# Kernel tuning notes

Hardware: AMD Instinct MI355X
Metric: run time of the kernel (lower is better)

The kernel has to match this reference:

```python
import jax, jax.numpy as jnp
import numpy as np

D_MODEL = 3072
NUM_EXPERTS = 8
TOP_K = 2
BATCH, SEQ = 4, 4096


def setup_inputs() -> dict:
    key = jax.random.key(0)
    kx, kw, kb = jax.random.split(key, 3)
    x = jax.random.normal(kx, (BATCH, SEQ, D_MODEL), dtype=jnp.float32)
    W = jax.random.normal(kw, (NUM_EXPERTS, D_MODEL), dtype=jnp.float32) * (1.0 / np.sqrt(D_MODEL))
    b = jax.random.normal(kb, (NUM_EXPERTS,), dtype=jnp.float32) * 0.02
    return {"x": x, "W": W, "b": b}


def reference(x, W, b):
    # Linear gate: [B, S, D] x [E, D]^T -> [B, S, E]
    logits = jnp.einsum("bsd,ed->bse", x, W) + b
    gate_scores = jax.nn.softmax(logits, axis=-1)
    # top-k over experts
    topk_values, topk_indices = jax.lax.top_k(gate_scores, TOP_K)
    # renormalize the selected scores with a second softmax
    topk_values = jax.nn.softmax(topk_values, axis=-1)
    return (topk_values, topk_indices)
```

## Files before the change

### kernel.cpp

```cpp
#include <hip/hip_runtime.h>
#include <stdint.h>


#define NTOK   16384
#define DMODEL 3072
#define NEXP   8
#define TPB    256
#define TOKB   16
#define NST    48
#define NSS    12

__global__ __launch_bounds__(TPB) void gate_fused_kernel(
    const float* __restrict__ x, const float* __restrict__ W,
    const float* __restrict__ bias, float* __restrict__ out) {
  const int tid = threadIdx.x;
  const int wv = tid >> 6;
  const int lane = tid & 63;
  const int tg = lane & 3;
  const int sl = lane >> 2;
  const int tok = blockIdx.x * TOKB + wv * 4 + tg;

  const float* px = x + (size_t)tok * DMODEL + sl * 4;
  const float* pw[NEXP];
#pragma unroll
  for (int e = 0; e < NEXP; ++e) pw[e] = W + (size_t)e * DMODEL + sl * 4;

  float acc[NEXP];
#pragma unroll
  for (int e = 0; e < NEXP; ++e) acc[e] = 0.f;

  float4 xa[4], xb[4];
#pragma unroll
  for (int k = 0; k < 4; ++k) xa[k] = *(const float4*)(px + k * 64);

#pragma unroll 1
  for (int ss = 0; ss < NSS; ss += 2) {
#pragma unroll
    for (int k = 0; k < 4; ++k)
      xb[k] = *(const float4*)(px + ((ss + 1) * 4 + k) * 64);

#pragma unroll
    for (int k = 0; k < 4; ++k) {
      const int s = ss * 4 + k;
      float4 w4[NEXP];
#pragma unroll
      for (int e = 0; e < NEXP; ++e)
        w4[e] = *(const float4*)(pw[e] + s * 64);
      const float4 xv = xa[k];
#pragma unroll
      for (int e = 0; e < NEXP; ++e)
        acc[e] = fmaf(xv.x, w4[e].x,
                 fmaf(xv.y, w4[e].y,
                 fmaf(xv.z, w4[e].z,
                 fmaf(xv.w, w4[e].w, acc[e]))));
    }

    if (ss + 2 < NSS) {
#pragma unroll
      for (int k = 0; k < 4; ++k)
        xa[k] = *(const float4*)(px + ((ss + 2) * 4 + k) * 64);
    }

#pragma unroll
    for (int k = 0; k < 4; ++k) {
      const int s = (ss + 1) * 4 + k;
      float4 w4[NEXP];
#pragma unroll
      for (int e = 0; e < NEXP; ++e)
        w4[e] = *(const float4*)(pw[e] + s * 64);
      const float4 xv = xb[k];
#pragma unroll
      for (int e = 0; e < NEXP; ++e)
        acc[e] = fmaf(xv.x, w4[e].x,
                 fmaf(xv.y, w4[e].y,
                 fmaf(xv.z, w4[e].z,
                 fmaf(xv.w, w4[e].w, acc[e]))));
    }
  }

#pragma unroll
  for (int e = 0; e < NEXP; ++e) {
    float v = acc[e];
    v += __shfl_xor(v, 4, 64);
    v += __shfl_xor(v, 8, 64);
    v += __shfl_xor(v, 16, 64);
    v += __shfl_xor(v, 32, 64);
    acc[e] = v;
  }

  const float4 b0 = *(const float4*)bias;
  const float4 b1 = *(const float4*)(bias + 4);
  float l[NEXP];
  l[0] = acc[0] + b0.x; l[1] = acc[1] + b0.y;
  l[2] = acc[2] + b0.z; l[3] = acc[3] + b0.w;
  l[4] = acc[4] + b1.x; l[5] = acc[5] + b1.y;
  l[6] = acc[6] + b1.z; l[7] = acc[7] + b1.w;

  float m = l[0];
#pragma unroll
  for (int e = 1; e < NEXP; ++e) m = fmaxf(m, l[e]);

  float p8[NEXP];
  float ssum = 0.f;
#pragma unroll
  for (int e = 0; e < NEXP; ++e) {
    p8[e] = expf(l[e] - m);
    ssum += p8[e];
  }
  const float inv = 1.f / ssum;
#pragma unroll
  for (int e = 0; e < NEXP; ++e) p8[e] *= inv;

  int i1 = 0;
  float v1 = p8[0];
#pragma unroll
  for (int e = 1; e < NEXP; ++e) {
    if (p8[e] > v1) { v1 = p8[e]; i1 = e; }
  }
  int i2 = -1;
  float v2 = -1.f;
#pragma unroll
  for (int e = 0; e < NEXP; ++e) {
    if (e == i1) continue;
    if (p8[e] > v2) { v2 = p8[e]; i2 = e; }
  }

  const float e2 = expf(v2 - v1);
  const float r = 1.f / (1.f + e2);

  if (lane < 4) {
    *(float2*)(out + (size_t)tok * 2) = make_float2(r, e2 * r);
    *(float2*)(out + 2 * NTOK + (size_t)tok * 2) =
        make_float2((float)i1, (float)i2);
  }
}

extern "C" void kernel_launch(void* const* d_in, const int* in_sizes, int n_in,
                              void* d_out, int out_size, void* d_ws,
                              size_t ws_size, hipStream_t stream) {
  const float* x = (const float*)d_in[0];
  const float* W = (const float*)d_in[1];
  const float* b = (const float*)d_in[2];
  float* out = (float*)d_out;
  (void)d_ws; (void)ws_size;

  gate_fused_kernel<<<dim3(NTOK / TOKB), TPB, 0, stream>>>(x, W, b, out);
}
```

Measured before the change: 307.2 us.

## Stage gate weights in double-buffered LDS and compute 8 tokens per wave

Weight chunks of 256 features for all 8 experts are now loaded cooperatively into double-buffered shared memory, with the next chunk prefetched while the current one is used. Each wave now processes 8 tokens instead of 4, and each thread accumulates four tokens, so every weight value read from LDS is reused across several tokens. This is meant to cut repeated global/L2 weight reads per token. In exchange it adds block barriers, more accumulator and x-prefetch registers, which may lower occupancy, and a longer shuffle reduction.

```diff
diff --git a/kernel.cpp b/kernel.cpp
--- a/kernel.cpp
+++ b/kernel.cpp
@@ -6,132 +6,173 @@
 #define DMODEL 3072
 #define NEXP   8
 #define TPB    256
-#define TOKB   16
-#define NST    48
-#define NSS    12
+#define TOKW   8
+#define TOKB   32
+#define CHF    256
+#define NCH    (DMODEL / CHF)
+#define LDSF   (NEXP * CHF)
 
-__global__ __launch_bounds__(TPB) void gate_fused_kernel(
+#define GATE_COMPUTE(SW, XR)                                          \
+  {                                                                   \
+    _Pragma("unroll")                                                 \
+    for (int st = 0; st < 2; ++st) {                                  \
+      float4 w4[NEXP];                                                \
+      _Pragma("unroll")                                               \
+      for (int e = 0; e < NEXP; ++e)                                  \
+        w4[e] = *(const float4*)&SW[e * CHF + st * 128 + sl * 4];     \
+      _Pragma("unroll")                                               \
+      for (int p = 0; p < 4; ++p) {                                   \
+        const float4 xv = XR[st * 4 + p];                             \
+        _Pragma("unroll")                                             \
+        for (int e = 0; e < NEXP; ++e)                                \
+          acc[p][e] = fmaf(xv.x, w4[e].x,                             \
+                      fmaf(xv.y, w4[e].y,                             \
+                      fmaf(xv.z, w4[e].z,                             \
+                      fmaf(xv.w, w4[e].w, acc[p][e]))));              \
+      }                                                               \
+    }                                                                 \
+  }
+
+__global__ __launch_bounds__(TPB) void gate_fused2(
     const float* __restrict__ x, const float* __restrict__ W,
     const float* __restrict__ bias, float* __restrict__ out) {
-  const int tid = threadIdx.x;
-  const int wv = tid >> 6;
+  __shared__ float swA[LDSF];
+  __shared__ float swB[LDSF];
+
+  const int tid  = threadIdx.x;
+  const int wv   = tid >> 6;
   const int lane = tid & 63;
-  const int tg = lane & 3;
-  const int sl = lane >> 2;
-  const int tok = blockIdx.x * TOKB + wv * 4 + tg;
+  const int tg   = lane & 1;
+  const int sl   = lane >> 1;
+  const int tokBase = blockIdx.x * TOKB + wv * TOKW;
 
-  const float* px = x + (size_t)tok * DMODEL + sl * 4;
-  const float* pw[NEXP];
+  const float* px[4];
 #pragma unroll
-  for (int e = 0; e < NEXP; ++e) pw[e] = W + (size_t)e * DMODEL + sl * 4;
+  for (int p = 0; p < 4; ++p)
+    px[p] = x + (size_t)(tokBase + p * 2 + tg) * DMODEL + sl * 4;
 
-  float acc[NEXP];
+  const float* pw0 = W + (size_t)wv * DMODEL + (tid & 63) * 4;
+  const float* pw1 = W + (size_t)(4 + wv) * DMODEL + (tid & 63) * 4;
+  const int d0 = tid * 4;
+  const int d1 = 1024 + tid * 4;
+
+  float acc[4][NEXP];
 #pragma unroll
-  for (int e = 0; e < NEXP; ++e) acc[e] = 0.f;
+  for (int p = 0; p < 4; ++p)
+#pragma unroll
+    for (int e = 0; e < NEXP; ++e) acc[p][e] = 0.f;
 
-  float4 xa[4], xb[4];
+  float4 w0 = *(const float4*)(pw0);
+  float4 w1 = *(const float4*)(pw1);
+  float4 xa[8], xb[8];
 #pragma unroll
-  for (int k = 0; k < 4; ++k) xa[k] = *(const float4*)(px + k * 64);
+  for (int st = 0; st < 2; ++st)
+#pragma unroll
+    for (int p = 0; p < 4; ++p)
+      xa[st * 4 + p] = *(const float4*)(px[p] + st * 128);
+  *(float4*)&swA[d0] = w0;
+  *(float4*)&swA[d1] = w1;
+  __syncthreads();
 
 #pragma unroll 1
-  for (int ss = 0; ss < NSS; ss += 2) {
+  for (int cc = 0; cc < NCH; cc += 2) {
+    w0 = *(const float4*)(pw0 + (cc + 1) * CHF);
+    w1 = *(const float4*)(pw1 + (cc + 1) * CHF);
 #pragma unroll
-    for (int k = 0; k < 4; ++k)
-      xb[k] = *(const float4*)(px + ((ss + 1) * 4 + k) * 64);
+    for (int st = 0; st < 2; ++st)
+#pragma unroll
+      for (int p = 0; p < 4; ++p)
+        xb[st * 4 + p] =
+            *(const float4*)(px[p] + ((cc + 1) * 2 + st) * 128);
 
+    GATE_COMPUTE(swA, xa);
+
+    *(float4*)&swB[d0] = w0;
+    *(float4*)&swB[d1] = w1;
+    __syncthreads();
+
+    if (cc + 2 < NCH) {
+      w0 = *(const float4*)(pw0 + (cc + 2) * CHF);
+      w1 = *(const float4*)(pw1 + (cc + 2) * CHF);
 #pragma unroll
-    for (int k = 0; k < 4; ++k) {
-      const int s = ss * 4 + k;
-      float4 w4[NEXP];
+      for (int st = 0; st < 2; ++st)
 #pragma unroll
-      for (int e = 0; e < NEXP; ++e)
-        w4[e] = *(const float4*)(pw[e] + s * 64);
-      const float4 xv = xa[k];
-#pragma unroll
-      for (int e = 0; e < NEXP; ++e)
-        acc[e] = fmaf(xv.x, w4[e].x,
-                 fmaf(xv.y, w4[e].y,
-                 fmaf(xv.z, w4[e].z,
-                 fmaf(xv.w, w4[e].w, acc[e]))));
+        for (int p = 0; p < 4; ++p)
+          xa[st * 4 + p] =
+              *(const float4*)(px[p] + ((cc + 2) * 2 + st) * 128);
     }
 
-    if (ss + 2 < NSS) {
-#pragma unroll
-      for (int k = 0; k < 4; ++k)
-        xa[k] = *(const float4*)(px + ((ss + 2) * 4 + k) * 64);
+    GATE_COMPUTE(swB, xb);
+
+    if (cc + 2 < NCH) {
+      *(float4*)&swA[d0] = w0;
+      *(float4*)&swA[d1] = w1;
     }
-
-#pragma unroll
-    for (int k = 0; k < 4; ++k) {
-      const int s = (ss + 1) * 4 + k;
-      float4 w4[NEXP];
-#pragma unroll
-      for (int e = 0; e < NEXP; ++e)
-        w4[e] = *(const float4*)(pw[e] + s * 64);
-      const float4 xv = xb[k];
-#pragma unroll
-      for (int e = 0; e < NEXP; ++e)
-        acc[e] = fmaf(xv.x, w4[e].x,
-                 fmaf(xv.y, w4[e].y,
-                 fmaf(xv.z, w4[e].z,
-                 fmaf(xv.w, w4[e].w, acc[e]))));
-    }
+    __syncthreads();
   }
 
 #pragma unroll
-  for (int e = 0; e < NEXP; ++e) {
-    float v = acc[e];
-    v += __shfl_xor(v, 4, 64);
-    v += __shfl_xor(v, 8, 64);
-    v += __shfl_xor(v, 16, 64);
-    v += __shfl_xor(v, 32, 64);
-    acc[e] = v;
-  }
+  for (int p = 0; p < 4; ++p)
+#pragma unroll
+    for (int e = 0; e < NEXP; ++e) {
+      float v = acc[p][e];
+      v += __shfl_xor(v, 2, 64);
+      v += __shfl_xor(v, 4, 64);
+      v += __shfl_xor(v, 8, 64);
+      v += __shfl_xor(v, 16, 64);
+      v += __shfl_xor(v, 32, 64);
+      acc[p][e] = v;
+    }
 
   const float4 b0 = *(const float4*)bias;
   const float4 b1 = *(const float4*)(bias + 4);
-  float l[NEXP];
-  l[0] = acc[0] + b0.x; l[1] = acc[1] + b0.y;
-  l[2] = acc[2] + b0.z; l[3] = acc[3] + b0.w;
-  l[4] = acc[4] + b1.x; l[5] = acc[5] + b1.y;
-  l[6] = acc[6] + b1.z; l[7] = acc[7] + b1.w;
 
-  float m = l[0];
 #pragma unroll
-  for (int e = 1; e < NEXP; ++e) m = fmaxf(m, l[e]);
+  for (int p = 0; p < 4; ++p) {
+    if (sl == p) {
+      float l[NEXP];
+      l[0] = acc[p][0] + b0.x; l[1] = acc[p][1] + b0.y;
+      l[2] = acc[p][2] + b0.z; l[3] = acc[p][3] + b0.w;
+      l[4] = acc[p][4] + b1.x; l[5] = acc[p][5] + b1.y;
+      l[6] = acc[p][6] + b1.z; l[7] = acc[p][7] + b1.w;
 
-  float p8[NEXP];
-  float ssum = 0.f;
+      float m = l[0];
 #pragma unroll
-  for (int e = 0; e < NEXP; ++e) {
-    p8[e] = expf(l[e] - m);
-    ssum += p8[e];
-  }
-  const float inv = 1.f / ssum;
+      for (int e = 1; e < NEXP; ++e) m = fmaxf(m, l[e]);
+
+      float p8[NEXP];
+      float ssum = 0.f;
 #pragma unroll
-  for (int e = 0; e < NEXP; ++e) p8[e] *= inv;
+      for (int e = 0; e < NEXP; ++e) {
+        p8[e] = expf(l[e] - m);
+        ssum += p8[e];
+      }
+      const float inv = 1.f / ssum;
+#pragma unroll
+      for (int e = 0; e < NEXP; ++e) p8[e] *= inv;
 
-  int i1 = 0;
-  float v1 = p8[0];
+      int i1 = 0;
+      float v1 = p8[0];
 #pragma unroll
-  for (int e = 1; e < NEXP; ++e) {
-    if (p8[e] > v1) { v1 = p8[e]; i1 = e; }
-  }
-  int i2 = -1;
-  float v2 = -1.f;
+      for (int e = 1; e < NEXP; ++e) {
+        if (p8[e] > v1) { v1 = p8[e]; i1 = e; }
+      }
+      int i2 = -1;
+      float v2 = -1.f;
 #pragma unroll
-  for (int e = 0; e < NEXP; ++e) {
-    if (e == i1) continue;
-    if (p8[e] > v2) { v2 = p8[e]; i2 = e; }
-  }
+      for (int e = 0; e < NEXP; ++e) {
+        if (e == i1) continue;
+        if (p8[e] > v2) { v2 = p8[e]; i2 = e; }
+      }
 
-  const float e2 = expf(v2 - v1);
-  const float r = 1.f / (1.f + e2);
+      const float e2 = expf(v2 - v1);
+      const float r = 1.f / (1.f + e2);
 
-  if (lane < 4) {
-    *(float2*)(out + (size_t)tok * 2) = make_float2(r, e2 * r);
-    *(float2*)(out + 2 * NTOK + (size_t)tok * 2) =
-        make_float2((float)i1, (float)i2);
+      const int tok = tokBase + p * 2 + tg;
+      *(float2*)(out + (size_t)tok * 2) = make_float2(r, e2 * r);
+      *(float2*)(out + 2 * NTOK + (size_t)tok * 2) =
+          make_float2((float)i1, (float)i2);
+    }
   }
 }
 
@@ -144,5 +185,5 @@
   float* out = (float*)d_out;
   (void)d_ws; (void)ws_size;
 
-  gate_fused_kernel<<<dim3(NTOK / TOKB), TPB, 0, stream>>>(x, W, b, out);
+  gate_fused2<<<dim3(NTOK / TOKB), TPB, 0, stream>>>(x, W, b, out);
 }
```

Result: faster. 293.1 us (-4.6%).

## Register-tile 8 tokens per wave and split experts across lane pairs

Applied to the files above, without the earlier changes.

Each wave now computes 8 tokens, with lane pairs splitting the 8 experts into two halves, so each W vector loaded is reused across 8 tokens instead of one. This cuts per-FMA load instructions and W cache traffic, which were heavy in the old one-token-per-lane-group layout. A lane-pair shuffle recombines the expert halves before softmax and top-k. It costs more registers for the accumulator tile, and x elements are loaded redundantly by both lanes of a pair.

```diff
diff --git a/kernel.cpp b/kernel.cpp
--- a/kernel.cpp
+++ b/kernel.cpp
@@ -6,129 +6,158 @@
 #define DMODEL 3072
 #define NEXP   8
 #define TPB    256
-#define TOKB   16
-#define NST    48
-#define NSS    12
+#define TOKW   8
+#define TOKB   32
+#define STF    128
+#define NST    (DMODEL / STF)
 
-__global__ __launch_bounds__(TPB) void gate_fused_kernel(
+#define GATE_COMPUTE(WR, XR)                                          \
+  {                                                                   \
+    _Pragma("unroll")                                                 \
+    for (int p = 0; p < TOKW; ++p) {                                  \
+      const float4 xv = XR[p];                                        \
+      _Pragma("unroll")                                               \
+      for (int e = 0; e < 4; ++e)                                     \
+        acc[p][e] = fmaf(xv.x, WR[e].x,                               \
+                    fmaf(xv.y, WR[e].y,                               \
+                    fmaf(xv.z, WR[e].z,                               \
+                    fmaf(xv.w, WR[e].w, acc[p][e]))));                \
+    }                                                                 \
+  }
+
+__global__ __launch_bounds__(TPB) void gate_fused3(
     const float* __restrict__ x, const float* __restrict__ W,
     const float* __restrict__ bias, float* __restrict__ out) {
-  const int tid = threadIdx.x;
-  const int wv = tid >> 6;
+  const int tid  = threadIdx.x;
+  const int wv   = tid >> 6;
   const int lane = tid & 63;
-  const int tg = lane & 3;
-  const int sl = lane >> 2;
-  const int tok = blockIdx.x * TOKB + wv * 4 + tg;
+  const int tg   = lane & 1;
+  const int sl   = lane >> 1;
+  const int tokBase = blockIdx.x * TOKB + wv * TOKW;
 
-  const float* px = x + (size_t)tok * DMODEL + sl * 4;
-  const float* pw[NEXP];
+  const float* px[TOKW];
 #pragma unroll
-  for (int e = 0; e < NEXP; ++e) pw[e] = W + (size_t)e * DMODEL + sl * 4;
+  for (int p = 0; p < TOKW; ++p)
+    px[p] = x + (size_t)(tokBase + p) * DMODEL + sl * 4;
 
-  float acc[NEXP];
+  const float* pw[4];
 #pragma unroll
-  for (int e = 0; e < NEXP; ++e) acc[e] = 0.f;
+  for (int e = 0; e < 4; ++e)
+    pw[e] = W + (size_t)(tg * 4 + e) * DMODEL + sl * 4;
 
-  float4 xa[4], xb[4];
+  float acc[TOKW][4];
 #pragma unroll
-  for (int k = 0; k < 4; ++k) xa[k] = *(const float4*)(px + k * 64);
+  for (int p = 0; p < TOKW; ++p)
+#pragma unroll
+    for (int e = 0; e < 4; ++e) acc[p][e] = 0.f;
+
+  float4 wa[4], wb[4], xa[TOKW], xb[TOKW];
+#pragma unroll
+  for (int e = 0; e < 4; ++e) wa[e] = *(const float4*)(pw[e]);
+#pragma unroll
+  for (int p = 0; p < TOKW; ++p) xa[p] = *(const float4*)(px[p]);
 
 #pragma unroll 1
-  for (int ss = 0; ss < NSS; ss += 2) {
+  for (int s = 0; s < NST; s += 2) {
 #pragma unroll
-    for (int k = 0; k < 4; ++k)
-      xb[k] = *(const float4*)(px + ((ss + 1) * 4 + k) * 64);
+    for (int e = 0; e < 4; ++e)
+      wb[e] = *(const float4*)(pw[e] + (s + 1) * STF);
+#pragma unroll
+    for (int p = 0; p < TOKW; ++p)
+      xb[p] = *(const float4*)(px[p] + (s + 1) * STF);
 
+    GATE_COMPUTE(wa, xa);
+
+    if (s + 2 < NST) {
 #pragma unroll
-    for (int k = 0; k < 4; ++k) {
-      const int s = ss * 4 + k;
-      float4 w4[NEXP];
+      for (int e = 0; e < 4; ++e)
+        wa[e] = *(const float4*)(pw[e] + (s + 2) * STF);
 #pragma unroll
-      for (int e = 0; e < NEXP; ++e)
-        w4[e] = *(const float4*)(pw[e] + s * 64);
-      const float4 xv = xa[k];
-#pragma unroll
-      for (int e = 0; e < NEXP; ++e)
-        acc[e] = fmaf(xv.x, w4[e].x,
-                 fmaf(xv.y, w4[e].y,
-                 fmaf(xv.z, w4[e].z,
-                 fmaf(xv.w, w4[e].w, acc[e]))));
+      for (int p = 0; p < TOKW; ++p)
+        xa[p] = *(const float4*)(px[p] + (s + 2) * STF);
     }
 
-    if (ss + 2 < NSS) {
-#pragma unroll
-      for (int k = 0; k < 4; ++k)
-        xa[k] = *(const float4*)(px + ((ss + 2) * 4 + k) * 64);
-    }
-
-#pragma unroll
-    for (int k = 0; k < 4; ++k) {
-      const int s = (ss + 1) * 4 + k;
-      float4 w4[NEXP];
-#pragma unroll
-      for (int e = 0; e < NEXP; ++e)
-        w4[e] = *(const float4*)(pw[e] + s * 64);
-      const float4 xv = xb[k];
-#pragma unroll
-      for (int e = 0; e < NEXP; ++e)
-        acc[e] = fmaf(xv.x, w4[e].x,
-                 fmaf(xv.y, w4[e].y,
-                 fmaf(xv.z, w4[e].z,
-                 fmaf(xv.w, w4[e].w, acc[e]))));
-    }
+    GATE_COMPUTE(wb, xb);
   }
 
 #pragma unroll
-  for (int e = 0; e < NEXP; ++e) {
-    float v = acc[e];
-    v += __shfl_xor(v, 4, 64);
-    v += __shfl_xor(v, 8, 64);
-    v += __shfl_xor(v, 16, 64);
-    v += __shfl_xor(v, 32, 64);
-    acc[e] = v;
+  for (int p = 0; p < TOKW; ++p)
+#pragma unroll
+    for (int e = 0; e < 4; ++e) {
+      float v = acc[p][e];
+      v += __shfl_xor(v, 2, 64);
+      v += __shfl_xor(v, 4, 64);
+      v += __shfl_xor(v, 8, 64);
+      v += __shfl_xor(v, 16, 64);
+      v += __shfl_xor(v, 32, 64);
+      acc[p][e] = v;
+    }
+
+  float own[4], send[4];
+#pragma unroll
+  for (int p = 0; p < TOKW; ++p) {
+    const bool isown  = (lane & 7) == p;
+    const bool issend = ((lane ^ 1) & 7) == p;
+#pragma unroll
+    for (int e = 0; e < 4; ++e) {
+      if (isown)  own[e]  = acc[p][e];
+      if (issend) send[e] = acc[p][e];
+    }
   }
+  float other[4];
+#pragma unroll
+  for (int e = 0; e < 4; ++e) other[e] = __shfl_xor(send[e], 1, 64);
 
-  const float4 b0 = *(const float4*)bias;
-  const float4 b1 = *(const float4*)(bias + 4);
-  float l[NEXP];
-  l[0] = acc[0] + b0.x; l[1] = acc[1] + b0.y;
-  l[2] = acc[2] + b0.z; l[3] = acc[3] + b0.w;
-  l[4] = acc[4] + b1.x; l[5] = acc[5] + b1.y;
-  l[6] = acc[6] + b1.z; l[7] = acc[7] + b1.w;
+  if (lane < TOKW) {
+    const float4 b0 = *(const float4*)bias;
+    const float4 b1 = *(const float4*)(bias + 4);
 
-  float m = l[0];
+    float l[NEXP];
+    if ((lane & 1) == 0) {
+      l[0] = own[0] + b0.x;   l[1] = own[1] + b0.y;
+      l[2] = own[2] + b0.z;   l[3] = own[3] + b0.w;
+      l[4] = other[0] + b1.x; l[5] = other[1] + b1.y;
+      l[6] = other[2] + b1.z; l[7] = other[3] + b1.w;
+    } else {
+      l[0] = other[0] + b0.x; l[1] = other[1] + b0.y;
+      l[2] = other[2] + b0.z; l[3] = other[3] + b0.w;
+      l[4] = own[0] + b1.x;   l[5] = own[1] + b1.y;
+      l[6] = own[2] + b1.z;   l[7] = own[3] + b1.w;
+    }
+
+    float m = l[0];
 #pragma unroll
-  for (int e = 1; e < NEXP; ++e) m = fmaxf(m, l[e]);
+    for (int e = 1; e < NEXP; ++e) m = fmaxf(m, l[e]);
 
-  float p8[NEXP];
-  float ssum = 0.f;
+    float p8[NEXP];
+    float ssum = 0.f;
 #pragma unroll
-  for (int e = 0; e < NEXP; ++e) {
-    p8[e] = expf(l[e] - m);
-    ssum += p8[e];
-  }
-  const float inv = 1.f / ssum;
+    for (int e = 0; e < NEXP; ++e) {
+      p8[e] = expf(l[e] - m);
+      ssum += p8[e];
+    }
+    const float inv = 1.f / ssum;
 #pragma unroll
-  for (int e = 0; e < NEXP; ++e) p8[e] *= inv;
+    for (int e = 0; e < NEXP; ++e) p8[e] *= inv;
 
-  int i1 = 0;
-  float v1 = p8[0];
+    int i1 = 0;
+    float v1 = p8[0];
 #pragma unroll
-  for (int e = 1; e < NEXP; ++e) {
-    if (p8[e] > v1) { v1 = p8[e]; i1 = e; }
-  }
-  int i2 = -1;
-  float v2 = -1.f;
+    for (int e = 1; e < NEXP; ++e) {
+      if (p8[e] > v1) { v1 = p8[e]; i1 = e; }
+    }
+    int i2 = -1;
+    float v2 = -1.f;
 #pragma unroll
-  for (int e = 0; e < NEXP; ++e) {
-    if (e == i1) continue;
-    if (p8[e] > v2) { v2 = p8[e]; i2 = e; }
-  }
+    for (int e = 0; e < NEXP; ++e) {
+      if (e == i1) continue;
+      if (p8[e] > v2) { v2 = p8[e]; i2 = e; }
+    }
 
-  const float e2 = expf(v2 - v1);
-  const float r = 1.f / (1.f + e2);
+    const float e2 = expf(v2 - v1);
+    const float r = 1.f / (1.f + e2);
 
-  if (lane < 4) {
+    const int tok = tokBase + lane;
     *(float2*)(out + (size_t)tok * 2) = make_float2(r, e2 * r);
     *(float2*)(out + 2 * NTOK + (size_t)tok * 2) =
         make_float2((float)i1, (float)i2);
@@ -144,5 +173,5 @@
   float* out = (float*)d_out;
   (void)d_ws; (void)ws_size;
 
-  gate_fused_kernel<<<dim3(NTOK / TOKB), TPB, 0, stream>>>(x, W, b, out);
+  gate_fused3<<<dim3(NTOK / TOKB), TPB, 0, stream>>>(x, W, b, out);
 }
```

Result: faster. 283.0 us (-7.9%).
